# Optimization experiments

Hardware: AMD Instinct MI355X
Metric: run time of the kernel (lower is better)

## Reference

```python
import jax, jax.numpy as jnp
import numpy as np

N_NODES = 50000
NEG_SLOPE = 0.2  # PyG GATConv default leaky-relu slope


def _gat_conv(x, edge_index, W, a_src, a_dst, bias, heads, out_ch, concat, num_nodes):
    # x: [N, F_in]; W: [F_in, heads*out_ch]; a_src/a_dst: [heads, out_ch]; bias: [heads*out_ch] or [out_ch]
    h = (x @ W).reshape(num_nodes, heads, out_ch)            # [N,H,C]
    alpha_src = jnp.einsum('nhc,hc->nh', h, a_src)           # [N,H]
    alpha_dst = jnp.einsum('nhc,hc->nh', h, a_dst)           # [N,H]
    src, dst = edge_index[0], edge_index[1]
    e = jax.nn.leaky_relu(alpha_src[src] + alpha_dst[dst], NEG_SLOPE)  # [E,H]
    # segment softmax over incoming edges per destination (self-loops guarantee non-empty segments)
    m = jax.ops.segment_max(e, dst, num_segments=num_nodes)
    e = jnp.exp(e - m[dst])
    denom = jax.ops.segment_sum(e, dst, num_segments=num_nodes)
    alpha = e / denom[dst]                                    # [E,H]
    msg = h[src] * alpha[:, :, None]                          # [E,H,C]
    out = jax.ops.segment_sum(msg, dst, num_segments=num_nodes)  # [N,H,C]
    if concat:
        out = out.reshape(num_nodes, heads * out_ch)
    else:
        out = out.mean(axis=1)
    return out + bias


def _add_self_loops(edge_index, num_nodes):
    loops = jnp.arange(num_nodes, dtype=edge_index.dtype)
    return jnp.concatenate([edge_index, jnp.stack([loops, loops])], axis=1)


def setup_inputs() -> dict:
    key = jax.random.key(0)
    ks = jax.random.split(key, 16)
    N, F_in, H, C_hid, C_out = N_NODES, 128, 4, 64, 64
    E = 800000
    x = jax.random.normal(ks[0], (N, F_in), dtype=jnp.float32)
    edge_index = jax.random.randint(ks[1], (2, E), 0, N, dtype=jnp.int32)
    s = lambda fan: 1.0 / np.sqrt(fan)
    inp = {
        'x': x, 'edge_index': edge_index,
        'W1': jax.random.normal(ks[2], (F_in, H * C_hid), jnp.float32) * s(F_in),
        'a_src1': jax.random.normal(ks[3], (H, C_hid), jnp.float32) * s(C_hid),
        'a_dst1': jax.random.normal(ks[4], (H, C_hid), jnp.float32) * s(C_hid),
        'b1': jnp.zeros((H * C_hid,), jnp.float32),
        'W2': jax.random.normal(ks[5], (H * C_hid, H * C_hid), jnp.float32) * s(H * C_hid),
        'a_src2': jax.random.normal(ks[6], (H, C_hid), jnp.float32) * s(C_hid),
        'a_dst2': jax.random.normal(ks[7], (H, C_hid), jnp.float32) * s(C_hid),
        'b2': jnp.zeros((H * C_hid,), jnp.float32),
        'W3': jax.random.normal(ks[8], (H * C_hid, C_out), jnp.float32) * s(H * C_hid),
        'a_src3': jax.random.normal(ks[9], (1, C_out), jnp.float32) * s(C_out),
        'a_dst3': jax.random.normal(ks[10], (1, C_out), jnp.float32) * s(C_out),
        'b3': jnp.zeros((C_out,), jnp.float32),
    }
    return inp


def reference(x, edge_index, W1, a_src1, a_dst1, b1, W2, a_src2, a_dst2, b2, W3, a_src3, a_dst3, b3):
    N = x.shape[0]
    ei = _add_self_loops(edge_index, N)
    h = _gat_conv(x, ei, W1, a_src1, a_dst1, b1, heads=4, out_ch=64, concat=True, num_nodes=N)
    h = jax.nn.elu(h)
    h = _gat_conv(h, ei, W2, a_src2, a_dst2, b2, heads=4, out_ch=64, concat=True, num_nodes=N)
    h = jax.nn.elu(h)
    out = _gat_conv(h, ei, W3, a_src3, a_dst3, b3, heads=1, out_ch=64, concat=False, num_nodes=N)
    return out
```

## Files before the change

### kernel.cpp

```cpp
#include <hip/hip_runtime.h>
#include <hip/hip_fp16.h>
#include <cstdint>


typedef _Float16 f16;
typedef _Float16 f16x8 __attribute__((ext_vector_type(8)));
typedef float f32x4 __attribute__((ext_vector_type(4)));

__global__ __launch_bounds__(256) void count_kernel(const int* __restrict__ ei,
                                                    int E, int N,
                                                    int* __restrict__ deg) {
  int g = blockIdx.x * 256 + threadIdx.x;
  if (g >= E + N) return;
  int dst = (g < E) ? ei[E + g] : (g - E);
  atomicAdd(&deg[dst], 1);
}

__global__ __launch_bounds__(256) void deg_block_reduce(const int* __restrict__ deg,
                                                        int* __restrict__ bsum, int N) {
  __shared__ int red[4];
  int b = blockIdx.x;
  int v = 0;
#pragma unroll
  for (int s = 0; s < 4; ++s) {
    int idx = b * 1024 + s * 256 + threadIdx.x;
    if (idx < N) v += deg[idx];
  }
  for (int off = 32; off; off >>= 1) v += __shfl_down(v, off);
  if ((threadIdx.x & 63) == 0) red[threadIdx.x >> 6] = v;
  __syncthreads();
  if (threadIdx.x == 0) bsum[b] = red[0] + red[1] + red[2] + red[3];
}

__global__ __launch_bounds__(1024) void small_scan(const int* __restrict__ bsum,
                                                   int* __restrict__ bpre, int NB) {
  __shared__ int buf[1024];
  int v = (threadIdx.x < NB) ? bsum[threadIdx.x] : 0;
  buf[threadIdx.x] = v;
  __syncthreads();
  for (int off = 1; off < 1024; off <<= 1) {
    int tv = (threadIdx.x >= off) ? buf[threadIdx.x - off] : 0;
    __syncthreads();
    buf[threadIdx.x] += tv;
    __syncthreads();
  }
  if (threadIdx.x < NB) bpre[threadIdx.x] = buf[threadIdx.x] - v;
}

__global__ __launch_bounds__(1024) void scan_final(const int* __restrict__ deg,
                                                   const int* __restrict__ bpre,
                                                   int* __restrict__ row_off,
                                                   int* __restrict__ cursor,
                                                   int N, int total) {
  __shared__ int buf[1024];
  int b = blockIdx.x;
  int i = b * 1024 + threadIdx.x;
  int v = (i < N) ? deg[i] : 0;
  buf[threadIdx.x] = v;
  __syncthreads();
  for (int off = 1; off < 1024; off <<= 1) {
    int tv = (threadIdx.x >= off) ? buf[threadIdx.x - off] : 0;
    __syncthreads();
    buf[threadIdx.x] += tv;
    __syncthreads();
  }
  if (i < N) {
    int ro = bpre[b] + buf[threadIdx.x] - v;
    row_off[i] = ro;
    cursor[i] = ro;
  }
  if (i == 0) row_off[N] = total;
}

__global__ __launch_bounds__(256) void scatter_kernel(const int* __restrict__ ei,
                                                      int E, int N,
                                                      int* __restrict__ cursor,
                                                      int* __restrict__ esrc,
                                                      int* __restrict__ edst) {
  int g = blockIdx.x * 256 + threadIdx.x;
  if (g >= E + N) return;
  int src, dst;
  if (g < E) { src = ei[g]; dst = ei[E + g]; }
  else       { src = g - E; dst = src; }
  int pos = atomicAdd(&cursor[dst], 1);
  esrc[pos] = src;
  edst[pos] = dst;
}

__global__ __launch_bounds__(256) void convert_wt(const float* __restrict__ W,
                                                  f16* __restrict__ Wt,
                                                  int K, int Ncol) {
  int t = blockIdx.x * 256 + threadIdx.x;
  if (t >= K * Ncol) return;
  int n = t % Ncol, k = t / Ncol;
  Wt[(size_t)n * K + k] = (f16)W[t];
}

template <int BN, bool ACAST>
__global__ __launch_bounds__(256) void mfma_gemm_alpha(
    const void* __restrict__ Ap_, const f16* __restrict__ Bt,
    f16* __restrict__ Tout,
    const float* __restrict__ avec_src, const float* __restrict__ avec_dst,
    float* __restrict__ asrc, float* __restrict__ adst,
    int M, int K, int Ncol) {
  constexpr int RF = (BN == 128) ? 4 : 2;
  __shared__ f16 As[128][40];
  __shared__ f16 Bs[BN][40];
  int tid = threadIdx.x;
  int wv = tid >> 6, lane = tid & 63;
  int lrow = lane & 15, lkb = lane >> 4;
  int row0 = blockIdx.x * 128, col0 = blockIdx.y * BN;
  int wro = (BN == 128) ? (wv >> 1) * 64 : wv * 32;
  int wco = (BN == 128) ? (wv & 1) * 64 : 0;
  int hg = (col0 + wco) >> 6;

  f32x4 acc[RF][4];
#pragma unroll
  for (int rf = 0; rf < RF; ++rf)
#pragma unroll
    for (int cf = 0; cf < 4; ++cf) acc[rf][cf] = (f32x4){0.f, 0.f, 0.f, 0.f};

  for (int kk = 0; kk < K; kk += 32) {
#pragma unroll
    for (int q = 0; q < 2; ++q) {
      int slot = tid + q * 256;
      int r = slot >> 2, ko = (slot & 3) << 3;
      int gr = min(row0 + r, M - 1);
      if (ACAST) {
        const float* Af = (const float*)Ap_ + (size_t)gr * K + kk + ko;
        float4 v0 = *reinterpret_cast<const float4*>(Af);
        float4 v1 = *reinterpret_cast<const float4*>(Af + 4);
        f16 o[8] = {(f16)v0.x, (f16)v0.y, (f16)v0.z, (f16)v0.w,
                    (f16)v1.x, (f16)v1.y, (f16)v1.z, (f16)v1.w};
        *reinterpret_cast<f16x8*>(&As[r][ko]) = *reinterpret_cast<f16x8*>(o);
      } else {
        *reinterpret_cast<f16x8*>(&As[r][ko]) =
            *reinterpret_cast<const f16x8*>((const f16*)Ap_ + (size_t)gr * K + kk + ko);
      }
    }
#pragma unroll
    for (int q = 0; q < BN / 64; ++q) {
      int slot = tid + q * 256;
      int c = slot >> 2, ko = (slot & 3) << 3;
      *reinterpret_cast<f16x8*>(&Bs[c][ko]) =
          *reinterpret_cast<const f16x8*>(&Bt[(size_t)(col0 + c) * K + kk + ko]);
    }
    __syncthreads();
    f16x8 af[RF], bf[4];
#pragma unroll
    for (int rf = 0; rf < RF; ++rf)
      af[rf] = *reinterpret_cast<f16x8*>(&As[wro + rf * 16 + lrow][lkb * 8]);
#pragma unroll
    for (int cf = 0; cf < 4; ++cf)
      bf[cf] = *reinterpret_cast<f16x8*>(&Bs[wco + cf * 16 + lrow][lkb * 8]);
#pragma unroll
    for (int rf = 0; rf < RF; ++rf)
#pragma unroll
      for (int cf = 0; cf < 4; ++cf)
        acc[rf][cf] = __builtin_amdgcn_mfma_f32_16x16x32_f16(af[rf], bf[cf],
                                                             acc[rf][cf], 0, 0, 0);
    __syncthreads();
  }

  int Hh = Ncol >> 6;
  float avs[4], avd[4];
#pragma unroll
  for (int cf = 0; cf < 4; ++cf) {
    avs[cf] = avec_src[hg * 64 + cf * 16 + lrow];
    avd[cf] = avec_dst[hg * 64 + cf * 16 + lrow];
  }

#pragma unroll
  for (int rf = 0; rf < RF; ++rf) {
#pragma unroll
    for (int r = 0; r < 4; ++r) {
      float ps = 0.f, pd = 0.f;
#pragma unroll
      for (int cf = 0; cf < 4; ++cf) {
        float v = acc[rf][cf][r];
        ps = fmaf(v, avs[cf], ps);
        pd = fmaf(v, avd[cf], pd);
      }
#pragma unroll
      for (int off = 1; off < 16; off <<= 1) {
        ps += __shfl_xor(ps, off);
        pd += __shfl_xor(pd, off);
      }
      int row = row0 + wro + rf * 16 + lkb * 4 + r;
      if (lrow == 0 && row < M) {
        asrc[row * Hh + hg] = ps;
        adst[row * Hh + hg] = pd;
      }
    }
#pragma unroll
    for (int r = 0; r < 4; ++r) {
      int row = row0 + wro + rf * 16 + lkb * 4 + r;
      if (row < M) {
#pragma unroll
        for (int cf = 0; cf < 4; ++cf)
          Tout[(size_t)row * Ncol + col0 + wco + cf * 16 + lrow] =
              (f16)acc[rf][cf][r];
      }
    }
  }
}

__global__ __launch_bounds__(256) void edge_weights_h4(
    const int* __restrict__ esrc, const int* __restrict__ edst,
    const float* __restrict__ asrc, const float* __restrict__ adst,
    float* __restrict__ w, int ET) {
  int t = blockIdx.x * 256 + threadIdx.x;
  if (t >= ET * 4) return;
  int j = t >> 2, h = t & 3;
  float e = asrc[esrc[j] * 4 + h] + adst[edst[j] * 4 + h];
  e = fmaxf(e, 0.2f * e);
  w[t] = __expf(e);
}

__global__ __launch_bounds__(256) void edge_weights_h1(
    const int* __restrict__ esrc, const int* __restrict__ edst,
    const float* __restrict__ asrc, const float* __restrict__ adst,
    float* __restrict__ w, int ET) {
  int j = blockIdx.x * 256 + threadIdx.x;
  if (j >= ET) return;
  float e = asrc[esrc[j]] + adst[edst[j]];
  e = fmaxf(e, 0.2f * e);
  w[j] = __expf(e);
}

template <bool ELU>
__global__ __launch_bounds__(256) void aggregate_h4(
    const f16* __restrict__ T16, const int* __restrict__ row_off,
    const int* __restrict__ esrc, const float* __restrict__ w,
    const float* __restrict__ bias, f16* __restrict__ outF, int N) {
  int wv = threadIdx.x >> 6, lane = threadIdx.x & 63;
  int dst = blockIdx.x * 4 + wv;
  if (dst >= N) return;
  int head = lane >> 4;
  int hsel = lane & 48;
  int ll = lane & 15;
  int r0 = row_off[dst], r1 = row_off[dst + 1];
  const char* tbase = reinterpret_cast<const char*>(T16);
  uint loff = (uint)lane * 8;
  float den = 0.f, ax = 0.f, ay = 0.f, az = 0.f, aw = 0.f;
  for (int base = r0; base < r1; base += 16) {
    int jb = base + ll;
    int sv = 0;
    float wl = 0.f;
    if (jb < r1) {
      sv = esrc[jb];
      wl = w[(jb << 2) + head];
    }
    int cnt = min(16, r1 - base);
#pragma unroll 4
    for (int i = 0; i < cnt; ++i) {
      int sj = __shfl(sv, i);
      float wj = __shfl(wl, hsel + i);
      den += wj;
      uint2 raw = *reinterpret_cast<const uint2*>(tbase + (((uint)sj << 9) + loff));
      __half2 p0 = *reinterpret_cast<__half2*>(&raw.x);
      __half2 p1 = *reinterpret_cast<__half2*>(&raw.y);
      float2 f0 = __half22float2(p0);
      float2 f1 = __half22float2(p1);
      ax = fmaf(wj, f0.x, ax);
      ay = fmaf(wj, f0.y, ay);
      az = fmaf(wj, f1.x, az);
      aw = fmaf(wj, f1.y, aw);
    }
  }
  float rd = 1.f / den;
  float4 bv = *reinterpret_cast<const float4*>(&bias[lane << 2]);
  float vx = ax * rd + bv.x, vy = ay * rd + bv.y;
  float vz = az * rd + bv.z, vw = aw * rd + bv.w;
  if (ELU) {
    vx = vx > 0.f ? vx : expm1f(vx);
    vy = vy > 0.f ? vy : expm1f(vy);
    vz = vz > 0.f ? vz : expm1f(vz);
    vw = vw > 0.f ? vw : expm1f(vw);
  }
  f16 o[4] = {(f16)vx, (f16)vy, (f16)vz, (f16)vw};
  *reinterpret_cast<uint2*>(&outF[(size_t)dst * 256 + (lane << 2)]) =
      *reinterpret_cast<uint2*>(o);
}

__global__ __launch_bounds__(256) void aggregate_h1(
    const f16* __restrict__ T16, const int* __restrict__ row_off,
    const int* __restrict__ esrc, const float* __restrict__ w,
    const float* __restrict__ bias, float* __restrict__ out, int N) {
  int wv = threadIdx.x >> 6, lane = threadIdx.x & 63;
  int grp = lane >> 4, l = lane & 15;
  int gsel = lane & 48;
  int dst = blockIdx.x * 16 + wv * 4 + grp;
  if (dst >= N) return;
  int r0 = row_off[dst], r1 = row_off[dst + 1];
  const char* tbase = reinterpret_cast<const char*>(T16);
  uint loff = (uint)l * 8;
  float den = 0.f, ax = 0.f, ay = 0.f, az = 0.f, aw = 0.f;
  for (int base = r0; base < r1; base += 16) {
    int jb = base + l;
    int sv = 0;
    float wl = 0.f;
    if (jb < r1) {
      sv = esrc[jb];
      wl = w[jb];
    }
    int cnt = min(16, r1 - base);
#pragma unroll 4
    for (int i = 0; i < cnt; ++i) {
      int sj = __shfl(sv, gsel + i);
      float wj = __shfl(wl, gsel + i);
      den += wj;
      uint2 raw = *reinterpret_cast<const uint2*>(tbase + (((uint)sj << 7) + loff));
      __half2 p0 = *reinterpret_cast<__half2*>(&raw.x);
      __half2 p1 = *reinterpret_cast<__half2*>(&raw.y);
      float2 f0 = __half22float2(p0);
      float2 f1 = __half22float2(p1);
      ax = fmaf(wj, f0.x, ax);
      ay = fmaf(wj, f0.y, ay);
      az = fmaf(wj, f1.x, az);
      aw = fmaf(wj, f1.y, aw);
    }
  }
  float rd = 1.f / den;
  float4 v;
  v.x = ax * rd + bias[l * 4 + 0];
  v.y = ay * rd + bias[l * 4 + 1];
  v.z = az * rd + bias[l * 4 + 2];
  v.w = aw * rd + bias[l * 4 + 3];
  *reinterpret_cast<float4*>(&out[(size_t)dst * 64 + l * 4]) = v;
}

extern "C" void kernel_launch(void* const* d_in, const int* in_sizes, int n_in,
                              void* d_out, int out_size, void* d_ws, size_t ws_size,
                              hipStream_t stream) {
  const float* x   = (const float*)d_in[0];
  const int*   ei  = (const int*)d_in[1];
  const float* W1  = (const float*)d_in[2];
  const float* as1 = (const float*)d_in[3];
  const float* ad1 = (const float*)d_in[4];
  const float* b1  = (const float*)d_in[5];
  const float* W2  = (const float*)d_in[6];
  const float* as2 = (const float*)d_in[7];
  const float* ad2 = (const float*)d_in[8];
  const float* b2  = (const float*)d_in[9];
  const float* W3  = (const float*)d_in[10];
  const float* as3 = (const float*)d_in[11];
  const float* ad3 = (const float*)d_in[12];
  const float* b3  = (const float*)d_in[13];
  float* out = (float*)d_out;

  const int Fin = 128, H = 4, C = 64, HC = H * C;
  const int N = in_sizes[0] / Fin;
  const int E = in_sizes[1] / 2;
  const int ET = E + N;
  const int NB = (N + 1023) / 1024;

  f16* T16   = (f16*)d_ws;
  f16* F16   = T16 + (size_t)N * HC;
  f16* T16L3 = F16 + (size_t)N * HC;
  f16* Wt1   = T16L3 + (size_t)N * C;
  f16* Wt2   = Wt1 + HC * Fin;
  f16* Wt3   = Wt2 + HC * HC;
  float* asrc = (float*)(Wt3 + C * HC);
  float* adst = asrc + (size_t)N * H;
  float* wbuf = adst + (size_t)N * H;
  int* deg     = (int*)(wbuf + (size_t)ET * 4);
  int* row_off = deg + N;
  int* cursor  = row_off + (N + 1);
  int* bsum    = cursor + N;
  int* bpre    = bsum + NB;
  int* esrc    = bpre + NB;
  int* edst    = esrc + ET;

  hipMemsetAsync(deg, 0, N * sizeof(int), stream);
  count_kernel<<<(ET + 255) / 256, 256, 0, stream>>>(ei, E, N, deg);
  deg_block_reduce<<<NB, 256, 0, stream>>>(deg, bsum, N);
  small_scan<<<1, 1024, 0, stream>>>(bsum, bpre, NB);
  scan_final<<<NB, 1024, 0, stream>>>(deg, bpre, row_off, cursor, N, ET);
  scatter_kernel<<<(ET + 255) / 256, 256, 0, stream>>>(ei, E, N, cursor, esrc, edst);

  convert_wt<<<(Fin * HC + 255) / 256, 256, 0, stream>>>(W1, Wt1, Fin, HC);
  convert_wt<<<(HC * HC + 255) / 256, 256, 0, stream>>>(W2, Wt2, HC, HC);
  convert_wt<<<(HC * C + 255) / 256, 256, 0, stream>>>(W3, Wt3, HC, C);

  int gx = (N + 127) / 128;
  int eb4 = (ET * 4 + 255) / 256, eb1 = (ET + 255) / 256;
  int ab4 = (N + 3) / 4;
  int ab1 = (N + 15) / 16;

  mfma_gemm_alpha<128, true><<<dim3(gx, 2), 256, 0, stream>>>(
      x, Wt1, T16, as1, ad1, asrc, adst, N, Fin, HC);
  edge_weights_h4<<<eb4, 256, 0, stream>>>(esrc, edst, asrc, adst, wbuf, ET);
  aggregate_h4<true><<<ab4, 256, 0, stream>>>(T16, row_off, esrc, wbuf, b1, F16, N);

  mfma_gemm_alpha<128, false><<<dim3(gx, 2), 256, 0, stream>>>(
      F16, Wt2, T16, as2, ad2, asrc, adst, N, HC, HC);
  edge_weights_h4<<<eb4, 256, 0, stream>>>(esrc, edst, asrc, adst, wbuf, ET);
  aggregate_h4<true><<<ab4, 256, 0, stream>>>(T16, row_off, esrc, wbuf, b2, F16, N);

  mfma_gemm_alpha<64, false><<<dim3(gx, 1), 256, 0, stream>>>(
      F16, Wt3, T16L3, as3, ad3, asrc, adst, N, HC, C);
  edge_weights_h1<<<eb1, 256, 0, stream>>>(esrc, edst, asrc, adst, wbuf, ET);
  aggregate_h1<<<ab1, 256, 0, stream>>>(T16L3, row_off, esrc, wbuf, b3, out, N);
}
```

Measured before the change: 368.3 us.

## Aggregate two destination nodes per wave with fixed 8-edge unrolled gathers

The 4-head aggregation kernel now has each wavefront process two destination nodes at once. Their neighbour-row gathers are interleaved in a fully unrolled 8-edge inner loop, so more independent loads are in flight. Padded slots reuse a valid source index with zero weight, and the loop runs to the larger of the two degrees, which wastes some work on the node with fewer edges. The single-head aggregation also moves to fixed, fully unrolled 8-edge chunks. The three weight-conversion launches are merged into one kernel to cut launch overhead.

```diff
diff --git a/kernel.cpp b/kernel.cpp
--- a/kernel.cpp
+++ b/kernel.cpp
@@ -87,13 +87,28 @@
   edst[pos] = dst;
 }
 
-__global__ __launch_bounds__(256) void convert_wt(const float* __restrict__ W,
-                                                  f16* __restrict__ Wt,
-                                                  int K, int Ncol) {
+__global__ __launch_bounds__(256) void convert_wt_all(
+    const float* __restrict__ W1, const float* __restrict__ W2,
+    const float* __restrict__ W3, f16* __restrict__ Wt1, f16* __restrict__ Wt2,
+    f16* __restrict__ Wt3, int n1, int n2, int n3, int N1, int N2, int N3,
+    int K1, int K2, int K3) {
   int t = blockIdx.x * 256 + threadIdx.x;
-  if (t >= K * Ncol) return;
-  int n = t % Ncol, k = t / Ncol;
-  Wt[(size_t)n * K + k] = (f16)W[t];
+  if (t < n1) {
+    int n = t % N1, k = t / N1;
+    Wt1[(size_t)n * K1 + k] = (f16)W1[t];
+    return;
+  }
+  t -= n1;
+  if (t < n2) {
+    int n = t % N2, k = t / N2;
+    Wt2[(size_t)n * K2 + k] = (f16)W2[t];
+    return;
+  }
+  t -= n2;
+  if (t < n3) {
+    int n = t % N3, k = t / N3;
+    Wt3[(size_t)n * K3 + k] = (f16)W3[t];
+  }
 }
 
 template <int BN, bool ACAST>
@@ -234,53 +249,90 @@
     const int* __restrict__ esrc, const float* __restrict__ w,
     const float* __restrict__ bias, f16* __restrict__ outF, int N) {
   int wv = threadIdx.x >> 6, lane = threadIdx.x & 63;
-  int dst = blockIdx.x * 4 + wv;
-  if (dst >= N) return;
+  int dst0 = blockIdx.x * 8 + wv * 2;
+  if (dst0 >= N) return;
+  bool has1 = (dst0 + 1 < N);
+  int dst1 = has1 ? dst0 + 1 : dst0;
   int head = lane >> 4;
-  int hsel = lane & 48;
-  int ll = lane & 15;
-  int r0 = row_off[dst], r1 = row_off[dst + 1];
+  int ds = lane >> 5, e4 = (lane >> 2) & 7, hh = lane & 3;
+  int r0a = row_off[dst0], r1a = row_off[dst0 + 1];
+  int r1b = row_off[dst1 + 1];
+  int r0b = row_off[dst1];
+  int sr0 = ds ? r0b : r0a, sr1 = ds ? r1b : r1a;
   const char* tbase = reinterpret_cast<const char*>(T16);
   uint loff = (uint)lane * 8;
-  float den = 0.f, ax = 0.f, ay = 0.f, az = 0.f, aw = 0.f;
-  for (int base = r0; base < r1; base += 16) {
-    int jb = base + ll;
-    int sv = 0;
-    float wl = 0.f;
-    if (jb < r1) {
+  float den0 = 0.f, den1 = 0.f;
+  float a0x = 0.f, a0y = 0.f, a0z = 0.f, a0w = 0.f;
+  float a1x = 0.f, a1y = 0.f, a1z = 0.f, a1w = 0.f;
+  int nb = max(r1a - r0a, r1b - r0b);
+  for (int base = 0; base < nb; base += 8) {
+    int jb = sr0 + base + e4;
+    int sv;
+    float wl;
+    if (jb < sr1) {
       sv = esrc[jb];
-      wl = w[(jb << 2) + head];
-    }
-    int cnt = min(16, r1 - base);
-#pragma unroll 4
-    for (int i = 0; i < cnt; ++i) {
-      int sj = __shfl(sv, i);
-      float wj = __shfl(wl, hsel + i);
-      den += wj;
-      uint2 raw = *reinterpret_cast<const uint2*>(tbase + (((uint)sj << 9) + loff));
-      __half2 p0 = *reinterpret_cast<__half2*>(&raw.x);
-      __half2 p1 = *reinterpret_cast<__half2*>(&raw.y);
-      float2 f0 = __half22float2(p0);
-      float2 f1 = __half22float2(p1);
-      ax = fmaf(wj, f0.x, ax);
-      ay = fmaf(wj, f0.y, ay);
-      az = fmaf(wj, f1.x, az);
-      aw = fmaf(wj, f1.y, aw);
-    }
-  }
-  float rd = 1.f / den;
+      wl = w[(jb << 2) + hh];
+    } else {
+      sv = esrc[sr1 - 1];
+      wl = 0.f;
+    }
+#pragma unroll
+    for (int i = 0; i < 8; ++i) {
+      int sj0 = __shfl(sv, i * 4);
+      float wj0 = __shfl(wl, i * 4 + head);
+      int sj1 = __shfl(sv, 32 + i * 4);
+      float wj1 = __shfl(wl, 32 + i * 4 + head);
+      uint2 raw0 = *reinterpret_cast<const uint2*>(tbase + (((uint)sj0 << 9) + loff));
+      uint2 raw1 = *reinterpret_cast<const uint2*>(tbase + (((uint)sj1 << 9) + loff));
+      den0 += wj0;
+      den1 += wj1;
+      __half2 q0 = *reinterpret_cast<__half2*>(&raw0.x);
+      __half2 q1 = *reinterpret_cast<__half2*>(&raw0.y);
+      float2 f0 = __half22float2(q0);
+      float2 f1 = __half22float2(q1);
+      a0x = fmaf(wj0, f0.x, a0x);
+      a0y = fmaf(wj0, f0.y, a0y);
+      a0z = fmaf(wj0, f1.x, a0z);
+      a0w = fmaf(wj0, f1.y, a0w);
+      __half2 q2 = *reinterpret_cast<__half2*>(&raw1.x);
+      __half2 q3 = *reinterpret_cast<__half2*>(&raw1.y);
+      float2 f2 = __half22float2(q2);
+      float2 f3 = __half22float2(q3);
+      a1x = fmaf(wj1, f2.x, a1x);
+      a1y = fmaf(wj1, f2.y, a1y);
+      a1z = fmaf(wj1, f3.x, a1z);
+      a1w = fmaf(wj1, f3.y, a1w);
+    }
+  }
   float4 bv = *reinterpret_cast<const float4*>(&bias[lane << 2]);
-  float vx = ax * rd + bv.x, vy = ay * rd + bv.y;
-  float vz = az * rd + bv.z, vw = aw * rd + bv.w;
-  if (ELU) {
-    vx = vx > 0.f ? vx : expm1f(vx);
-    vy = vy > 0.f ? vy : expm1f(vy);
-    vz = vz > 0.f ? vz : expm1f(vz);
-    vw = vw > 0.f ? vw : expm1f(vw);
-  }
-  f16 o[4] = {(f16)vx, (f16)vy, (f16)vz, (f16)vw};
-  *reinterpret_cast<uint2*>(&outF[(size_t)dst * 256 + (lane << 2)]) =
-      *reinterpret_cast<uint2*>(o);
+  {
+    float rd = 1.f / den0;
+    float vx = a0x * rd + bv.x, vy = a0y * rd + bv.y;
+    float vz = a0z * rd + bv.z, vw = a0w * rd + bv.w;
+    if (ELU) {
+      vx = vx > 0.f ? vx : expm1f(vx);
+      vy = vy > 0.f ? vy : expm1f(vy);
+      vz = vz > 0.f ? vz : expm1f(vz);
+      vw = vw > 0.f ? vw : expm1f(vw);
+    }
+    f16 o[4] = {(f16)vx, (f16)vy, (f16)vz, (f16)vw};
+    *reinterpret_cast<uint2*>(&outF[(size_t)dst0 * 256 + (lane << 2)]) =
+        *reinterpret_cast<uint2*>(o);
+  }
+  if (has1) {
+    float rd = 1.f / den1;
+    float vx = a1x * rd + bv.x, vy = a1y * rd + bv.y;
+    float vz = a1z * rd + bv.z, vw = a1w * rd + bv.w;
+    if (ELU) {
+      vx = vx > 0.f ? vx : expm1f(vx);
+      vy = vy > 0.f ? vy : expm1f(vy);
+      vz = vz > 0.f ? vz : expm1f(vz);
+      vw = vw > 0.f ? vw : expm1f(vw);
+    }
+    f16 o[4] = {(f16)vx, (f16)vy, (f16)vz, (f16)vw};
+    *reinterpret_cast<uint2*>(&outF[(size_t)dst1 * 256 + (lane << 2)]) =
+        *reinterpret_cast<uint2*>(o);
+  }
 }
 
 __global__ __launch_bounds__(256) void aggregate_h1(
@@ -296,17 +348,16 @@
   const char* tbase = reinterpret_cast<const char*>(T16);
   uint loff = (uint)l * 8;
   float den = 0.f, ax = 0.f, ay = 0.f, az = 0.f, aw = 0.f;
-  for (int base = r0; base < r1; base += 16) {
-    int jb = base + l;
+  for (int base = r0; base < r1; base += 8) {
+    int jb = base + (l & 7);
     int sv = 0;
     float wl = 0.f;
     if (jb < r1) {
       sv = esrc[jb];
       wl = w[jb];
     }
-    int cnt = min(16, r1 - base);
-#pragma unroll 4
-    for (int i = 0; i < cnt; ++i) {
+#pragma unroll
+    for (int i = 0; i < 8; ++i) {
       int sj = __shfl(sv, gsel + i);
       float wj = __shfl(wl, gsel + i);
       den += wj;
@@ -379,13 +430,13 @@
   scan_final<<<NB, 1024, 0, stream>>>(deg, bpre, row_off, cursor, N, ET);
   scatter_kernel<<<(ET + 255) / 256, 256, 0, stream>>>(ei, E, N, cursor, esrc, edst);
 
-  convert_wt<<<(Fin * HC + 255) / 256, 256, 0, stream>>>(W1, Wt1, Fin, HC);
-  convert_wt<<<(HC * HC + 255) / 256, 256, 0, stream>>>(W2, Wt2, HC, HC);
-  convert_wt<<<(HC * C + 255) / 256, 256, 0, stream>>>(W3, Wt3, HC, C);
+  int n1 = Fin * HC, n2 = HC * HC, n3 = HC * C;
+  convert_wt_all<<<(n1 + n2 + n3 + 255) / 256, 256, 0, stream>>>(
+      W1, W2, W3, Wt1, Wt2, Wt3, n1, n2, n3, HC, HC, C, Fin, HC, HC);
 
   int gx = (N + 127) / 128;
   int eb4 = (ET * 4 + 255) / 256, eb1 = (ET + 255) / 256;
-  int ab4 = (N + 3) / 4;
+  int ab4 = (N + 7) / 8;
   int ab1 = (N + 15) / 16;
 
   mfma_gemm_alpha<128, true><<<dim3(gx, 2), 256, 0, stream>>>(
```

Measured after the change: 358.1 us. -2.8%, faster.
